# Performance work log

Measured on AMD Instinct MI355X. Metric: run time of the kernel, lower is better.

## Reference

```python
import jax, jax.numpy as jnp
import numpy as np

NUM_CLASSES = 1000  # label vocabulary size (matches fill_max for label)
B = 16384
D_IN = 1024   # image_embedding
D_OUT = 256   # projection_dim


def setup_inputs() -> dict:
    key = jax.random.key(0)
    k = jax.random.split(key, 6)
    x = jax.random.normal(k[0], (B, D_IN), dtype=jnp.float32)
    label = jax.random.randint(k[1], (B,), 0, NUM_CLASSES, dtype=jnp.int64)
    scale = 1.0 / np.sqrt(D_IN)
    W1_w = jax.random.normal(k[2], (D_OUT, D_IN), dtype=jnp.float32) * scale
    W1_b = jax.random.normal(k[3], (D_OUT,), dtype=jnp.float32) * scale
    W2_w = jax.random.normal(k[4], (D_OUT, D_IN), dtype=jnp.float32) * scale
    W2_b = jax.random.normal(k[5], (D_OUT,), dtype=jnp.float32) * scale
    return {"x": x, "label": label, "W1_w": W1_w, "W1_b": W1_b,
            "W2_w": W2_w, "W2_b": W2_b}


def reference(x, label, W1_w, W1_b, W2_w, W2_b):
    # Leave-one-group-out mean, vectorized via segment sums.
    # Original: for each i, mean of x[label != label_i] (detached); zeros if none.
    b = x.shape[0]
    xd = jax.lax.stop_gradient(x)  # .detach() in the torch code
    label_sum = jax.ops.segment_sum(xd, label, num_segments=NUM_CLASSES)          # [C, D_IN]
    label_cnt = jax.ops.segment_sum(jnp.ones((b,), dtype=x.dtype), label,
                                    num_segments=NUM_CLASSES)                     # [C]
    total_sum = xd.sum(axis=0)                                                    # [D_IN]
    other_sum = total_sum[None, :] - label_sum[label]                             # [B, D_IN]
    other_cnt = jnp.asarray(b, x.dtype) - label_cnt[label]                        # [B]
    calculate_mean = jnp.where(other_cnt[:, None] > 0,
                               other_sum / jnp.maximum(other_cnt, 1)[:, None],
                               jnp.zeros((), x.dtype))                            # [B, D_IN]
    # W1(x) + W2(calculate_mean)  (torch Linear: y = x @ W.T + b)
    return x @ W1_w.T + W1_b + calculate_mean @ W2_w.T + W2_b
```

## Files before the change

### kernel.cpp

```cpp
#include <hip/hip_runtime.h>
#include <hip/hip_bf16.h>

constexpr int B      = 16384;
constexpr int D_IN   = 1024;
constexpr int D_OUT  = 256;
constexpr int NCLS   = 1000;
constexpr int CPAD   = 1024;

constexpr size_t OFF_XB   = 0;
constexpr size_t OFF_WB   = OFF_XB  + (size_t)B * D_IN * 2;
constexpr size_t OFF_S    = OFF_WB  + (size_t)512 * D_IN * 2;
constexpr size_t OFF_Z    = OFF_S   + (size_t)CPAD * D_IN * 4;
constexpr size_t OFF_T    = OFF_Z   + (size_t)CPAD * D_OUT * 4;
constexpr size_t OFF_CNT  = OFF_T   + (size_t)D_IN * 4;
constexpr size_t OFF_OFFS = OFF_CNT + (size_t)CPAD * 4;
constexpr size_t OFF_CUR  = OFF_OFFS+ (size_t)CPAD * 4;
constexpr size_t OFF_ROWL = OFF_CUR + (size_t)CPAD * 4;

typedef short bf16x8 __attribute__((ext_vector_type(8)));
typedef float f32x4  __attribute__((ext_vector_type(4)));

__device__ __forceinline__ unsigned short f2bf(float f) {
    unsigned int u = __float_as_uint(f);
    return (unsigned short)((u + 0x7FFFu + ((u >> 16) & 1u)) >> 16);
}

__device__ __forceinline__ void cvt8(const float4& a, const float4& b, unsigned short* dst) {
    union { unsigned short u[8]; bf16x8 v; } r;
    r.u[0] = f2bf(a.x); r.u[1] = f2bf(a.y); r.u[2] = f2bf(a.z); r.u[3] = f2bf(a.w);
    r.u[4] = f2bf(b.x); r.u[5] = f2bf(b.y); r.u[6] = f2bf(b.z); r.u[7] = f2bf(b.w);
    *(bf16x8*)dst = r.v;
}

__device__ __forceinline__ ushort4 f2bf4(const float4& a) {
    ushort4 r;
    r.x = f2bf(a.x); r.y = f2bf(a.y); r.z = f2bf(a.z); r.w = f2bf(a.w);
    return r;
}

__device__ __forceinline__ void async16(const unsigned short* g, unsigned short* l) {
    __builtin_amdgcn_global_load_lds(
        (const __attribute__((address_space(1))) void*)g,
        (__attribute__((address_space(3))) void*)l,
        16, 0, 0);
}

__global__ __launch_bounds__(1024)
void prep_kernel(const float* __restrict__ W1, const float* __restrict__ W2,
                 unsigned short* __restrict__ Wb,
                 float* __restrict__ T, float* __restrict__ Z,
                 const int* __restrict__ label,
                 int* __restrict__ cnt, int* __restrict__ offs,
                 int* __restrict__ rowlist) {
    __shared__ int hA[1024];
    __shared__ int hB[1024];

    if (blockIdx.x < 64) {
        int lin = blockIdx.x * 1024 + threadIdx.x;
        int i = lin * 8;
        const float* src = (i < D_OUT * D_IN) ? (W1 + i) : (W2 + (i - D_OUT * D_IN));
        float4 a = *(const float4*)(src);
        float4 b = *(const float4*)(src + 4);
        cvt8(a, b, Wb + i);
        if (lin < D_IN) T[lin] = 0.f;
        *(float4*)(Z + (size_t)lin * 4) = float4{0.f, 0.f, 0.f, 0.f};
        return;
    }

    int t = threadIdx.x;
    hA[t] = 0;
    __syncthreads();
    int lab[16];
#pragma unroll
    for (int r = 0; r < 16; ++r) {
        lab[r] = label[t + r * 1024];
        atomicAdd(&hA[lab[r]], 1);
    }
    __syncthreads();
    int v = hA[t];
    int* src = hA;
    int* dst = hB;
    for (int off = 1; off < 1024; off <<= 1) {
        int sv = src[t];
        if (t >= off) sv += src[t - off];
        dst[t] = sv;
        __syncthreads();
        int* tmp = src; src = dst; dst = tmp;
    }
    int excl = src[t] - v;
    cnt[t]  = v;
    offs[t] = excl;
    dst[t]  = excl;
    __syncthreads();
#pragma unroll
    for (int r = 0; r < 16; ++r) {
        int p = atomicAdd(&dst[lab[r]], 1);
        rowlist[p] = t + r * 1024;
    }
}

__global__ __launch_bounds__(128)
void segsum_kernel(const float* __restrict__ x,
                   const int* __restrict__ offs,
                   const int* __restrict__ cnt,
                   const int* __restrict__ rowlist,
                   float* __restrict__ s,
                   unsigned short* __restrict__ xb) {
    int c = blockIdx.x;
    int col = blockIdx.y * 512 + threadIdx.x * 4;
    float4 acc = {0.f, 0.f, 0.f, 0.f};
    if (c < NCLS) {
        int o = offs[c], n = cnt[c];
        int r = 0;
        for (; r + 8 <= n; r += 8) {
            int idx[8];
#pragma unroll
            for (int u = 0; u < 8; ++u) idx[u] = rowlist[o + r + u];
            float4 v[8];
#pragma unroll
            for (int u = 0; u < 8; ++u)
                v[u] = *(const float4*)(x + (size_t)idx[u] * D_IN + col);
#pragma unroll
            for (int u = 0; u < 8; ++u)
                *(ushort4*)(xb + (size_t)idx[u] * D_IN + col) = f2bf4(v[u]);
#pragma unroll
            for (int u = 0; u < 8; ++u) {
                acc.x += v[u].x; acc.y += v[u].y; acc.z += v[u].z; acc.w += v[u].w;
            }
        }
        for (; r + 4 <= n; r += 4) {
            int i0 = rowlist[o + r + 0];
            int i1 = rowlist[o + r + 1];
            int i2 = rowlist[o + r + 2];
            int i3 = rowlist[o + r + 3];
            float4 v0 = *(const float4*)(x + (size_t)i0 * D_IN + col);
            float4 v1 = *(const float4*)(x + (size_t)i1 * D_IN + col);
            float4 v2 = *(const float4*)(x + (size_t)i2 * D_IN + col);
            float4 v3 = *(const float4*)(x + (size_t)i3 * D_IN + col);
            *(ushort4*)(xb + (size_t)i0 * D_IN + col) = f2bf4(v0);
            *(ushort4*)(xb + (size_t)i1 * D_IN + col) = f2bf4(v1);
            *(ushort4*)(xb + (size_t)i2 * D_IN + col) = f2bf4(v2);
            *(ushort4*)(xb + (size_t)i3 * D_IN + col) = f2bf4(v3);
            acc.x += (v0.x + v1.x) + (v2.x + v3.x);
            acc.y += (v0.y + v1.y) + (v2.y + v3.y);
            acc.z += (v0.z + v1.z) + (v2.z + v3.z);
            acc.w += (v0.w + v1.w) + (v2.w + v3.w);
        }
        for (; r < n; ++r) {
            int i0 = rowlist[o + r];
            float4 v = *(const float4*)(x + (size_t)i0 * D_IN + col);
            *(ushort4*)(xb + (size_t)i0 * D_IN + col) = f2bf4(v);
            acc.x += v.x; acc.y += v.y; acc.z += v.z; acc.w += v.w;
        }
    }
    *(float4*)(s + (size_t)c * D_IN + col) = acc;
}

__global__ void tsum_kernel(const float* __restrict__ s, float* __restrict__ T) {
    int col = threadIdx.x * 4;
    int c0 = blockIdx.x * 16;
    float4 acc = {0.f, 0.f, 0.f, 0.f};
#pragma unroll 4
    for (int c = 0; c < 16; ++c) {
        float4 v = *(const float4*)(s + (size_t)(c0 + c) * D_IN + col);
        acc.x += v.x; acc.y += v.y; acc.z += v.z; acc.w += v.w;
    }
    atomicAdd(&T[col + 0], acc.x);
    atomicAdd(&T[col + 1], acc.y);
    atomicAdd(&T[col + 2], acc.z);
    atomicAdd(&T[col + 3], acc.w);
}

__global__ __launch_bounds__(256)
void meanz_kernel(const float* __restrict__ s,
                  const float* __restrict__ T,
                  const int* __restrict__ cnt,
                  const unsigned short* __restrict__ Wb,
                  const float* __restrict__ b2,
                  float* __restrict__ Z) {
    __shared__ unsigned short As[2][64 * 32];
    __shared__ unsigned short Bs[2][64 * 32];

    const int tid  = threadIdx.x;
    const int wave = tid >> 6;
    const int lane = tid & 63;
    const int quad = lane >> 4;
    const int l16  = lane & 15;
    const int bm   = blockIdx.x * 64;
    const int bn   = blockIdx.y * 64;
    const int kb   = blockIdx.z * 256;
    const int wm   = (wave >> 1) * 32;
    const int wn   = (wave & 1) * 32;

    const int arow = tid >> 2;
    const int akc  = (tid & 3) * 8;

    const int cls = bm + arow;
    const int d   = B - cnt[cls];
    const float scale = (d > 0) ? 1.f / (float)d : 0.f;
    const float* sp = s + (size_t)cls * D_IN + akc;
    const float* tp = T + akc;

    const int bidx = wave * 64 + lane;
    const int brow = bidx >> 2;
    const int bkc  = (bidx & 3) * 8;
    const unsigned short* bp = Wb + (size_t)(256 + bn + brow) * D_IN + bkc;

    f32x4 acc[2][2] = {};

    float4 cs0 = *(const float4*)(sp + kb);
    float4 cs1 = *(const float4*)(sp + kb + 4);
    float4 ct0 = *(const float4*)(tp + kb);
    float4 ct1 = *(const float4*)(tp + kb + 4);
    async16(bp + kb, Bs[0] + wave * 512);

    for (int it = 0; it < 8; ++it) {
        const int cur = it & 1;
        const int k0  = kb + it * 32;
        float4 m0 = {(ct0.x - cs0.x) * scale, (ct0.y - cs0.y) * scale,
                     (ct0.z - cs0.z) * scale, (ct0.w - cs0.w) * scale};
        float4 m1 = {(ct1.x - cs1.x) * scale, (ct1.y - cs1.y) * scale,
                     (ct1.z - cs1.z) * scale, (ct1.w - cs1.w) * scale};
        cvt8(m0, m1, As[cur] + arow * 32 + akc);
        if (it < 7) {
            async16(bp + k0 + 32, Bs[cur ^ 1] + wave * 512);
            cs0 = *(const float4*)(sp + k0 + 32);
            cs1 = *(const float4*)(sp + k0 + 36);
            ct0 = *(const float4*)(tp + k0 + 32);
            ct1 = *(const float4*)(tp + k0 + 36);
        }
        __syncthreads();

        bf16x8 af[2], bfr[2];
#pragma unroll
        for (int t = 0; t < 2; ++t) {
            af[t]  = *(const bf16x8*)&As[cur][(wm + t * 16 + l16) * 32 + quad * 8];
            bfr[t] = *(const bf16x8*)&Bs[cur][(wn + t * 16 + l16) * 32 + quad * 8];
        }
#pragma unroll
        for (int i = 0; i < 2; ++i)
#pragma unroll
            for (int j = 0; j < 2; ++j)
                acc[i][j] = __builtin_amdgcn_mfma_f32_16x16x32_bf16(af[i], bfr[j], acc[i][j], 0, 0, 0);
    }

    const bool addb = (blockIdx.z == 0);
#pragma unroll
    for (int j = 0; j < 2; ++j) {
        const int n = bn + wn + j * 16 + l16;
        const float bias = addb ? b2[n] : 0.f;
#pragma unroll
        for (int i = 0; i < 2; ++i)
#pragma unroll
            for (int r = 0; r < 4; ++r) {
                const int c = bm + wm + i * 16 + quad * 4 + r;
                atomicAdd(&Z[(size_t)c * D_OUT + n], acc[i][j][r] + bias);
            }
    }
}

__global__ __launch_bounds__(256)
void gemm1_kernel(const unsigned short* __restrict__ xb,
                  const unsigned short* __restrict__ Wb,
                  const float* __restrict__ b1,
                  const float* __restrict__ Z,
                  const int* __restrict__ label,
                  float* __restrict__ out) {
    __shared__ unsigned short As[2][2][128][32];
    __shared__ unsigned short Bs[2][2][64][32];

    const int tid  = threadIdx.x;
    const int wave = tid >> 6;
    const int lane = tid & 63;
    const int quad = lane >> 4;
    const int l16  = lane & 15;
    const int bm   = blockIdx.x * 128;
    const int bn   = blockIdx.y * 64;
    const int wm   = (wave >> 1) * 64;
    const int wn   = (wave & 1) * 32;

    const unsigned short* aps[4];
#pragma unroll
    for (int rr = 0; rr < 4; ++rr) {
        int dd = rr * 256 + tid;
        int h = dd >> 9, r = (dd >> 2) & 127, c = dd & 3;
        aps[rr] = xb + (size_t)(bm + r) * D_IN + h * 32 + c * 8;
    }
    const unsigned short* bps[2];
#pragma unroll
    for (int rr = 0; rr < 2; ++rr) {
        int dd = rr * 256 + tid;
        int h = dd >> 8, r = (dd >> 2) & 63, c = dd & 3;
        bps[rr] = Wb + (size_t)(bn + r) * D_IN + h * 32 + c * 8;
    }

    f32x4 acc[4][2] = {};

    {
        unsigned short* ab = &As[0][0][0][0];
        unsigned short* bb = &Bs[0][0][0][0];
#pragma unroll
        for (int rr = 0; rr < 4; ++rr) async16(aps[rr], ab + rr * 2048 + wave * 512);
#pragma unroll
        for (int rr = 0; rr < 2; ++rr) async16(bps[rr], bb + rr * 2048 + wave * 512);
    }
    __syncthreads();

    for (int t = 0; t < 16; ++t) {
        const int cur = t & 1;
        if (t + 1 < 16) {
            const int k1 = (t + 1) * 64;
            unsigned short* ab = &As[cur ^ 1][0][0][0];
            unsigned short* bb = &Bs[cur ^ 1][0][0][0];
#pragma unroll
            for (int rr = 0; rr < 4; ++rr) async16(aps[rr] + k1, ab + rr * 2048 + wave * 512);
#pragma unroll
            for (int rr = 0; rr < 2; ++rr) async16(bps[rr] + k1, bb + rr * 2048 + wave * 512);
        }

#pragma unroll
        for (int ks = 0; ks < 2; ++ks) {
            bf16x8 af[4], bfr[2];
#pragma unroll
            for (int i = 0; i < 4; ++i)
                af[i] = *(const bf16x8*)&As[cur][ks][wm + i * 16 + l16][quad * 8];
#pragma unroll
            for (int j = 0; j < 2; ++j)
                bfr[j] = *(const bf16x8*)&Bs[cur][ks][wn + j * 16 + l16][quad * 8];
#pragma unroll
            for (int i = 0; i < 4; ++i)
#pragma unroll
                for (int j = 0; j < 2; ++j)
                    acc[i][j] = __builtin_amdgcn_mfma_f32_16x16x32_bf16(af[i], bfr[j], acc[i][j], 0, 0, 0);
        }
        __syncthreads();
    }

    int zrow[4][4];
#pragma unroll
    for (int i = 0; i < 4; ++i)
#pragma unroll
        for (int r = 0; r < 4; ++r)
            zrow[i][r] = label[bm + wm + i * 16 + quad * 4 + r] * D_OUT;

#pragma unroll
    for (int j = 0; j < 2; ++j) {
        const int n = bn + wn + j * 16 + l16;
        const float bias = b1[n];
#pragma unroll
        for (int i = 0; i < 4; ++i)
#pragma unroll
            for (int r = 0; r < 4; ++r) {
                const int m = bm + wm + i * 16 + quad * 4 + r;
                out[(size_t)m * D_OUT + n] = acc[i][j][r] + bias + Z[zrow[i][r] + n];
            }
    }
}

extern "C" void kernel_launch(void* const* d_in, const int* in_sizes, int n_in,
                              void* d_out, int out_size, void* d_ws, size_t ws_size,
                              hipStream_t stream) {
    const float* x    = (const float*)d_in[0];
    const int*   lab  = (const int*)d_in[1];
    const float* W1_w = (const float*)d_in[2];
    const float* W1_b = (const float*)d_in[3];
    const float* W2_w = (const float*)d_in[4];
    const float* W2_b = (const float*)d_in[5];
    float* out = (float*)d_out;

    char* ws = (char*)d_ws;
    unsigned short* xb = (unsigned short*)(ws + OFF_XB);
    unsigned short* Wb = (unsigned short*)(ws + OFF_WB);
    float* s   = (float*)(ws + OFF_S);
    float* Z   = (float*)(ws + OFF_Z);
    float* T   = (float*)(ws + OFF_T);
    int* cnt     = (int*)(ws + OFF_CNT);
    int* offs    = (int*)(ws + OFF_OFFS);
    int* rowlist = (int*)(ws + OFF_ROWL);

    prep_kernel<<<65, 1024, 0, stream>>>(W1_w, W2_w, Wb, T, Z, lab, cnt, offs, rowlist);
    dim3 sgrid(CPAD, 2);
    segsum_kernel<<<sgrid, 128, 0, stream>>>(x, offs, cnt, rowlist, s, xb);
    tsum_kernel<<<64, 256, 0, stream>>>(s, T);
    dim3 zgrid(CPAD / 64, D_OUT / 64, 4);
    meanz_kernel<<<zgrid, 256, 0, stream>>>(s, T, cnt, Wb, W2_b, Z);
    dim3 ggrid(B / 128, D_OUT / 64);
    gemm1_kernel<<<ggrid, 256, 0, stream>>>(xb, Wb, W1_b, Z, lab, out);
}
```

Before: 164.4 us.

## Fuse all stages into one cooperative persistent kernel with grid syncs

```diff
diff --git a/kernel.cpp b/kernel.cpp
--- a/kernel.cpp
+++ b/kernel.cpp
@@ -1,5 +1,7 @@
 #include <hip/hip_runtime.h>
-#include <hip/hip_bf16.h>
+#include <hip/hip_cooperative_groups.h>
+
+namespace cg = cooperative_groups;
 
 constexpr int B      = 16384;
 constexpr int D_IN   = 1024;
@@ -45,120 +47,104 @@
         16, 0, 0);
 }
 
-__global__ __launch_bounds__(1024)
-void prep_kernel(const float* __restrict__ W1, const float* __restrict__ W2,
-                 unsigned short* __restrict__ Wb,
-                 float* __restrict__ T, float* __restrict__ Z,
-                 const int* __restrict__ label,
-                 int* __restrict__ cnt, int* __restrict__ offs,
-                 int* __restrict__ rowlist) {
-    __shared__ int hA[1024];
-    __shared__ int hB[1024];
-
-    if (blockIdx.x < 64) {
-        int lin = blockIdx.x * 1024 + threadIdx.x;
+
+__device__ __forceinline__ void phase_prep(int blk, int tid, char* smem,
+    const float* __restrict__ W1w, const float* __restrict__ W2w,
+    unsigned short* __restrict__ Wb, float* __restrict__ T, float* __restrict__ Z,
+    const int* __restrict__ label, int* __restrict__ cnt, int* __restrict__ offs,
+    int* __restrict__ rowlist)
+{
+    if (blk < 256) {
+        int lin = blk * 256 + tid;
         int i = lin * 8;
-        const float* src = (i < D_OUT * D_IN) ? (W1 + i) : (W2 + (i - D_OUT * D_IN));
+        const float* src = (i < D_OUT * D_IN) ? (W1w + i) : (W2w + (i - D_OUT * D_IN));
         float4 a = *(const float4*)(src);
         float4 b = *(const float4*)(src + 4);
         cvt8(a, b, Wb + i);
         if (lin < D_IN) T[lin] = 0.f;
         *(float4*)(Z + (size_t)lin * 4) = float4{0.f, 0.f, 0.f, 0.f};
-        return;
-    }
-
-    int t = threadIdx.x;
-    hA[t] = 0;
-    __syncthreads();
-    int lab[16];
-#pragma unroll
-    for (int r = 0; r < 16; ++r) {
-        lab[r] = label[t + r * 1024];
-        atomicAdd(&hA[lab[r]], 1);
-    }
-    __syncthreads();
-    int v = hA[t];
-    int* src = hA;
-    int* dst = hB;
-    for (int off = 1; off < 1024; off <<= 1) {
-        int sv = src[t];
-        if (t >= off) sv += src[t - off];
-        dst[t] = sv;
-        __syncthreads();
-        int* tmp = src; src = dst; dst = tmp;
-    }
-    int excl = src[t] - v;
-    cnt[t]  = v;
-    offs[t] = excl;
-    dst[t]  = excl;
-    __syncthreads();
-#pragma unroll
-    for (int r = 0; r < 16; ++r) {
-        int p = atomicAdd(&dst[lab[r]], 1);
-        rowlist[p] = t + r * 1024;
-    }
-}
-
-__global__ __launch_bounds__(128)
-void segsum_kernel(const float* __restrict__ x,
-                   const int* __restrict__ offs,
-                   const int* __restrict__ cnt,
-                   const int* __restrict__ rowlist,
-                   float* __restrict__ s,
-                   unsigned short* __restrict__ xb) {
-    int c = blockIdx.x;
-    int col = blockIdx.y * 512 + threadIdx.x * 4;
-    float4 acc = {0.f, 0.f, 0.f, 0.f};
-    if (c < NCLS) {
-        int o = offs[c], n = cnt[c];
-        int r = 0;
-        for (; r + 8 <= n; r += 8) {
-            int idx[8];
-#pragma unroll
-            for (int u = 0; u < 8; ++u) idx[u] = rowlist[o + r + u];
-            float4 v[8];
-#pragma unroll
-            for (int u = 0; u < 8; ++u)
-                v[u] = *(const float4*)(x + (size_t)idx[u] * D_IN + col);
-#pragma unroll
-            for (int u = 0; u < 8; ++u)
-                *(ushort4*)(xb + (size_t)idx[u] * D_IN + col) = f2bf4(v[u]);
-#pragma unroll
-            for (int u = 0; u < 8; ++u) {
-                acc.x += v[u].x; acc.y += v[u].y; acc.z += v[u].z; acc.w += v[u].w;
+    } else if (blk == 256) {
+        int* hA = (int*)smem;
+        int* hB = hA + 1024;
+#pragma unroll
+        for (int q = 0; q < 4; ++q) hA[q * 256 + tid] = 0;
+        __syncthreads();
+        for (int r = 0; r < 64; ++r)
+            atomicAdd(&hA[label[r * 256 + tid]], 1);
+        __syncthreads();
+        int v0 = hA[tid * 4 + 0], v1 = hA[tid * 4 + 1];
+        int v2 = hA[tid * 4 + 2], v3 = hA[tid * 4 + 3];
+        int s1 = v0 + v1, s2 = s1 + v2, s3 = s2 + v3;
+        hB[tid] = s3;
+        __syncthreads();
+        for (int off = 1; off < 256; off <<= 1) {
+            int mine = hB[tid];
+            int add  = (tid >= off) ? hB[tid - off] : 0;
+            __syncthreads();
+            hB[tid] = mine + add;
+            __syncthreads();
+        }
+        int ex = hB[tid] - s3;
+        cnt[tid * 4 + 0] = v0; cnt[tid * 4 + 1] = v1;
+        cnt[tid * 4 + 2] = v2; cnt[tid * 4 + 3] = v3;
+        int e0 = ex, e1 = ex + v0, e2 = ex + s1, e3 = ex + s2;
+        offs[tid * 4 + 0] = e0; offs[tid * 4 + 1] = e1;
+        offs[tid * 4 + 2] = e2; offs[tid * 4 + 3] = e3;
+        hA[tid * 4 + 0] = e0; hA[tid * 4 + 1] = e1;
+        hA[tid * 4 + 2] = e2; hA[tid * 4 + 3] = e3;
+        __syncthreads();
+        for (int r = 0; r < 64; ++r) {
+            int i0 = r * 256 + tid;
+            int p = atomicAdd(&hA[label[i0]], 1);
+            rowlist[p] = i0;
+        }
+    }
+}
+
+__device__ __forceinline__ void phase_segsum(int blk, int tid,
+    const float* __restrict__ x, const int* __restrict__ offs,
+    const int* __restrict__ cnt, const int* __restrict__ rowlist,
+    float* __restrict__ s, unsigned short* __restrict__ xb)
+{
+    int col = tid * 4;
+    for (int c = blk * 2; c < blk * 2 + 2; ++c) {
+        float4 acc = {0.f, 0.f, 0.f, 0.f};
+        if (c < NCLS) {
+            int o = offs[c], n = cnt[c];
+            int r = 0;
+            for (; r + 8 <= n; r += 8) {
+                int idx[8];
+#pragma unroll
+                for (int u = 0; u < 8; ++u) idx[u] = rowlist[o + r + u];
+                float4 v[8];
+#pragma unroll
+                for (int u = 0; u < 8; ++u)
+                    v[u] = *(const float4*)(x + (size_t)idx[u] * D_IN + col);
+#pragma unroll
+                for (int u = 0; u < 8; ++u)
+                    *(ushort4*)(xb + (size_t)idx[u] * D_IN + col) = f2bf4(v[u]);
+#pragma unroll
+                for (int u = 0; u < 8; ++u) {
+                    acc.x += v[u].x; acc.y += v[u].y; acc.z += v[u].z; acc.w += v[u].w;
+                }
             }
-        }
-        for (; r + 4 <= n; r += 4) {
-            int i0 = rowlist[o + r + 0];
-            int i1 = rowlist[o + r + 1];
-            int i2 = rowlist[o + r + 2];
-            int i3 = rowlist[o + r + 3];
-            float4 v0 = *(const float4*)(x + (size_t)i0 * D_IN + col);
-            float4 v1 = *(const float4*)(x + (size_t)i1 * D_IN + col);
-            float4 v2 = *(const float4*)(x + (size_t)i2 * D_IN + col);
-            float4 v3 = *(const float4*)(x + (size_t)i3 * D_IN + col);
-            *(ushort4*)(xb + (size_t)i0 * D_IN + col) = f2bf4(v0);
-            *(ushort4*)(xb + (size_t)i1 * D_IN + col) = f2bf4(v1);
-            *(ushort4*)(xb + (size_t)i2 * D_IN + col) = f2bf4(v2);
-            *(ushort4*)(xb + (size_t)i3 * D_IN + col) = f2bf4(v3);
-            acc.x += (v0.x + v1.x) + (v2.x + v3.x);
-            acc.y += (v0.y + v1.y) + (v2.y + v3.y);
-            acc.z += (v0.z + v1.z) + (v2.z + v3.z);
-            acc.w += (v0.w + v1.w) + (v2.w + v3.w);
-        }
-        for (; r < n; ++r) {
-            int i0 = rowlist[o + r];
-            float4 v = *(const float4*)(x + (size_t)i0 * D_IN + col);
-            *(ushort4*)(xb + (size_t)i0 * D_IN + col) = f2bf4(v);
-            acc.x += v.x; acc.y += v.y; acc.z += v.z; acc.w += v.w;
-        }
-    }
-    *(float4*)(s + (size_t)c * D_IN + col) = acc;
-}
-
-__global__ void tsum_kernel(const float* __restrict__ s, float* __restrict__ T) {
-    int col = threadIdx.x * 4;
-    int c0 = blockIdx.x * 16;
+            for (; r < n; ++r) {
+                int i0 = rowlist[o + r];
+                float4 v = *(const float4*)(x + (size_t)i0 * D_IN + col);
+                *(ushort4*)(xb + (size_t)i0 * D_IN + col) = f2bf4(v);
+                acc.x += v.x; acc.y += v.y; acc.z += v.z; acc.w += v.w;
+            }
+        }
+        *(float4*)(s + (size_t)c * D_IN + col) = acc;
+    }
+}
+
+__device__ __forceinline__ void phase_tsum(int blk, int tid,
+    const float* __restrict__ s, float* __restrict__ T)
+{
+    if (blk >= 64) return;
+    int col = tid * 4;
+    int c0 = blk * 16;
     float4 acc = {0.f, 0.f, 0.f, 0.f};
 #pragma unroll 4
     for (int c = 0; c < 16; ++c) {
@@ -171,29 +157,20 @@
     atomicAdd(&T[col + 3], acc.w);
 }
 
-__global__ __launch_bounds__(256)
-void meanz_kernel(const float* __restrict__ s,
-                  const float* __restrict__ T,
-                  const int* __restrict__ cnt,
-                  const unsigned short* __restrict__ Wb,
-                  const float* __restrict__ b2,
-                  float* __restrict__ Z) {
-    __shared__ unsigned short As[2][64 * 32];
-    __shared__ unsigned short Bs[2][64 * 32];
-
-    const int tid  = threadIdx.x;
-    const int wave = tid >> 6;
-    const int lane = tid & 63;
-    const int quad = lane >> 4;
-    const int l16  = lane & 15;
-    const int bm   = blockIdx.x * 64;
-    const int bn   = blockIdx.y * 64;
-    const int kb   = blockIdx.z * 256;
-    const int wm   = (wave >> 1) * 32;
-    const int wn   = (wave & 1) * 32;
-
-    const int arow = tid >> 2;
-    const int akc  = (tid & 3) * 8;
+__device__ __forceinline__ void phase_meanz(int blk, int tid, char* smem,
+    const float* __restrict__ s, const float* __restrict__ T,
+    const int* __restrict__ cnt, const unsigned short* __restrict__ Wb,
+    const float* __restrict__ b2, float* __restrict__ Z)
+{
+    unsigned short* mAs = (unsigned short*)smem;
+    unsigned short* mBs = mAs + 2 * 2048;
+
+    const int wave = tid >> 6, lane = tid & 63;
+    const int quad = lane >> 4, l16 = lane & 15;
+    const int mt = blk & 15, nt = (blk >> 4) & 3, kt = blk >> 6;
+    const int bm = mt * 64, bn = nt * 64, kb = kt * 128;
+    const int wm = (wave >> 1) * 32, wn = (wave & 1) * 32;
+    const int arow = tid >> 2, akc = (tid & 3) * 8;
 
     const int cls = bm + arow;
     const int d   = B - cnt[cls];
@@ -202,8 +179,7 @@
     const float* tp = T + akc;
 
     const int bidx = wave * 64 + lane;
-    const int brow = bidx >> 2;
-    const int bkc  = (bidx & 3) * 8;
+    const int brow = bidx >> 2, bkc = (bidx & 3) * 8;
     const unsigned short* bp = Wb + (size_t)(256 + bn + brow) * D_IN + bkc;
 
     f32x4 acc[2][2] = {};
@@ -212,30 +188,31 @@
     float4 cs1 = *(const float4*)(sp + kb + 4);
     float4 ct0 = *(const float4*)(tp + kb);
     float4 ct1 = *(const float4*)(tp + kb + 4);
-    async16(bp + kb, Bs[0] + wave * 512);
-
-    for (int it = 0; it < 8; ++it) {
+    async16(bp + kb, mBs + wave * 512);
+
+    for (int it = 0; it < 4; ++it) {
         const int cur = it & 1;
         const int k0  = kb + it * 32;
         float4 m0 = {(ct0.x - cs0.x) * scale, (ct0.y - cs0.y) * scale,
                      (ct0.z - cs0.z) * scale, (ct0.w - cs0.w) * scale};
         float4 m1 = {(ct1.x - cs1.x) * scale, (ct1.y - cs1.y) * scale,
                      (ct1.z - cs1.z) * scale, (ct1.w - cs1.w) * scale};
-        cvt8(m0, m1, As[cur] + arow * 32 + akc);
-        if (it < 7) {
-            async16(bp + k0 + 32, Bs[cur ^ 1] + wave * 512);
+        cvt8(m0, m1, mAs + cur * 2048 + arow * 32 + akc);
+        if (it < 3) {
             cs0 = *(const float4*)(sp + k0 + 32);
             cs1 = *(const float4*)(sp + k0 + 36);
             ct0 = *(const float4*)(tp + k0 + 32);
             ct1 = *(const float4*)(tp + k0 + 36);
         }
         __syncthreads();
+        if (it < 3)
+            async16(bp + k0 + 32, mBs + (cur ^ 1) * 2048 + wave * 512);
 
         bf16x8 af[2], bfr[2];
 #pragma unroll
-        for (int t = 0; t < 2; ++t) {
-            af[t]  = *(const bf16x8*)&As[cur][(wm + t * 16 + l16) * 32 + quad * 8];
-            bfr[t] = *(const bf16x8*)&Bs[cur][(wn + t * 16 + l16) * 32 + quad * 8];
+        for (int t2 = 0; t2 < 2; ++t2) {
+            af[t2]  = *(const bf16x8*)&mAs[cur * 2048 + (wm + t2 * 16 + l16) * 32 + quad * 8];
+            bfr[t2] = *(const bf16x8*)&mBs[cur * 2048 + (wn + t2 * 16 + l16) * 32 + quad * 8];
         }
 #pragma unroll
         for (int i = 0; i < 2; ++i)
@@ -244,7 +221,7 @@
                 acc[i][j] = __builtin_amdgcn_mfma_f32_16x16x32_bf16(af[i], bfr[j], acc[i][j], 0, 0, 0);
     }
 
-    const bool addb = (blockIdx.z == 0);
+    const bool addb = (kt == 0);
 #pragma unroll
     for (int j = 0; j < 2; ++j) {
         const int n = bn + wn + j * 16 + l16;
@@ -259,25 +236,21 @@
     }
 }
 
-__global__ __launch_bounds__(256)
-void gemm1_kernel(const unsigned short* __restrict__ xb,
-                  const unsigned short* __restrict__ Wb,
-                  const float* __restrict__ b1,
-                  const float* __restrict__ Z,
-                  const int* __restrict__ label,
-                  float* __restrict__ out) {
-    __shared__ unsigned short As[2][2][128][32];
-    __shared__ unsigned short Bs[2][2][64][32];
-
-    const int tid  = threadIdx.x;
-    const int wave = tid >> 6;
-    const int lane = tid & 63;
-    const int quad = lane >> 4;
-    const int l16  = lane & 15;
-    const int bm   = blockIdx.x * 128;
-    const int bn   = blockIdx.y * 64;
-    const int wm   = (wave >> 1) * 64;
-    const int wn   = (wave & 1) * 32;
+__device__ __forceinline__ void phase_gemm1(int blk, int tid, char* smem,
+    const unsigned short* __restrict__ xb, const unsigned short* __restrict__ Wb,
+    const float* __restrict__ b1, const float* __restrict__ Z,
+    const int* __restrict__ label, float* __restrict__ out)
+{
+    typedef unsigned short (*AsT)[2][128][32];
+    typedef unsigned short (*BsT)[2][64][32];
+    AsT As = (AsT)smem;
+    BsT Bs = (BsT)(smem + 32768);
+
+    const int wave = tid >> 6, lane = tid & 63;
+    const int quad = lane >> 4, l16 = lane & 15;
+    const int bx = blk & 127, by = blk >> 7;
+    const int bm = bx * 128, bn = by * 64;
+    const int wm = (wave >> 1) * 64, wn = (wave & 1) * 32;
 
     const unsigned short* aps[4];
 #pragma unroll
@@ -317,7 +290,6 @@
 #pragma unroll
             for (int rr = 0; rr < 2; ++rr) async16(bps[rr] + k1, bb + rr * 2048 + wave * 512);
         }
-
 #pragma unroll
         for (int ks = 0; ks < 2; ++ks) {
             bf16x8 af[4], bfr[2];
@@ -355,6 +327,56 @@
                 out[(size_t)m * D_OUT + n] = acc[i][j][r] + bias + Z[zrow[i][r] + n];
             }
     }
+}
+
+__global__ __launch_bounds__(256, 2)
+void mega_kernel(const float* __restrict__ x, const int* __restrict__ label,
+                 const float* __restrict__ W1w, const float* __restrict__ b1,
+                 const float* __restrict__ W2w, const float* __restrict__ b2,
+                 float* __restrict__ out,
+                 unsigned short* __restrict__ xb, unsigned short* __restrict__ Wb,
+                 float* __restrict__ s, float* __restrict__ Z, float* __restrict__ T,
+                 int* __restrict__ cnt, int* __restrict__ offs, int* __restrict__ rowlist)
+{
+    cg::grid_group grid = cg::this_grid();
+    __shared__ __align__(16) char smem[49152];
+    const int tid = threadIdx.x;
+    const int blk = blockIdx.x;
+
+    phase_prep(blk, tid, smem, W1w, W2w, Wb, T, Z, label, cnt, offs, rowlist);
+    grid.sync();
+    phase_segsum(blk, tid, x, offs, cnt, rowlist, s, xb);
+    grid.sync();
+    phase_tsum(blk, tid, s, T);
+    grid.sync();
+    phase_meanz(blk, tid, smem, s, T, cnt, Wb, b2, Z);
+    grid.sync();
+    phase_gemm1(blk, tid, smem, xb, Wb, b1, Z, label, out);
+}
+
+__global__ __launch_bounds__(256) void prep_fb(const float* W1w, const float* W2w,
+    unsigned short* Wb, float* T, float* Z, const int* label,
+    int* cnt, int* offs, int* rowlist) {
+    __shared__ __align__(16) char smem[16384];
+    phase_prep(blockIdx.x, threadIdx.x, smem, W1w, W2w, Wb, T, Z, label, cnt, offs, rowlist);
+}
+__global__ __launch_bounds__(256) void segsum_fb(const float* x, const int* offs,
+    const int* cnt, const int* rowlist, float* s, unsigned short* xb) {
+    phase_segsum(blockIdx.x, threadIdx.x, x, offs, cnt, rowlist, s, xb);
+}
+__global__ __launch_bounds__(256) void tsum_fb(const float* s, float* T) {
+    phase_tsum(blockIdx.x, threadIdx.x, s, T);
+}
+__global__ __launch_bounds__(256) void meanz_fb(const float* s, const float* T,
+    const int* cnt, const unsigned short* Wb, const float* b2, float* Z) {
+    __shared__ __align__(16) char smem[16384];
+    phase_meanz(blockIdx.x, threadIdx.x, smem, s, T, cnt, Wb, b2, Z);
+}
+__global__ __launch_bounds__(256) void gemm1_fb(const unsigned short* xb,
+    const unsigned short* Wb, const float* b1, const float* Z,
+    const int* label, float* out) {
+    __shared__ __align__(16) char smem[49152];
+    phase_gemm1(blockIdx.x, threadIdx.x, smem, xb, Wb, b1, Z, label, out);
 }
 
 extern "C" void kernel_launch(void* const* d_in, const int* in_sizes, int n_in,
@@ -378,12 +400,19 @@
     int* offs    = (int*)(ws + OFF_OFFS);
     int* rowlist = (int*)(ws + OFF_ROWL);
 
-    prep_kernel<<<65, 1024, 0, stream>>>(W1_w, W2_w, Wb, T, Z, lab, cnt, offs, rowlist);
-    dim3 sgrid(CPAD, 2);
-    segsum_kernel<<<sgrid, 128, 0, stream>>>(x, offs, cnt, rowlist, s, xb);
-    tsum_kernel<<<64, 256, 0, stream>>>(s, T);
-    dim3 zgrid(CPAD / 64, D_OUT / 64, 4);
-    meanz_kernel<<<zgrid, 256, 0, stream>>>(s, T, cnt, Wb, W2_b, Z);
-    dim3 ggrid(B / 128, D_OUT / 64);
-    gemm1_kernel<<<ggrid, 256, 0, stream>>>(xb, Wb, W1_b, Z, lab, out);
-}
+    void* args[] = { (void*)&x, (void*)&lab, (void*)&W1_w, (void*)&W1_b,
+                     (void*)&W2_w, (void*)&W2_b, (void*)&out,
+                     (void*)&xb, (void*)&Wb, (void*)&s, (void*)&Z, (void*)&T,
+                     (void*)&cnt, (void*)&offs, (void*)&rowlist };
+
+    hipError_t err = hipLaunchCooperativeKernel(mega_kernel, dim3(512), dim3(256),
+                                                args, 0, stream);
+    if (err != hipSuccess) {
+        (void)hipGetLastError();
+        prep_fb<<<257, 256, 0, stream>>>(W1_w, W2_w, Wb, T, Z, lab, cnt, offs, rowlist);
+        segsum_fb<<<512, 256, 0, stream>>>(x, offs, cnt, rowlist, s, xb);
+        tsum_fb<<<64, 256, 0, stream>>>(s, T);
+        meanz_fb<<<512, 256, 0, stream>>>(s, T, cnt, Wb, W2_b, Z);
+        gemm1_fb<<<512, 256, 0, stream>>>(xb, Wb, W1_b, Z, lab, out);
+    }
+}
```

Result: slower. 402.9 us (+145.1%).
